# Kernel tuning notes

Measured on AMD Instinct MI355X. Metric: run time of the kernel, lower is better.

## Reference

```python
import jax, jax.numpy as jnp
import numpy as np

NUM_HEADS = 16
EMBED_DIM = 1024
HEAD_DIM = EMBED_DIM // NUM_HEADS


def setup_inputs() -> dict:
    key = jax.random.key(0)
    ks = jax.random.split(key, 9)
    B, S, D = 4, 2048, EMBED_DIM
    scale = 1.0 / np.sqrt(D)
    inp = {
        "x": jax.random.normal(ks[0], (B, S, D), dtype=jnp.float32),
        "Wq": jax.random.normal(ks[1], (D, D), dtype=jnp.float32) * scale,
        "bq": jnp.zeros((D,), dtype=jnp.float32),
        "Wk": jax.random.normal(ks[2], (D, D), dtype=jnp.float32) * scale,
        "bk": jnp.zeros((D,), dtype=jnp.float32),
        "Wv": jax.random.normal(ks[3], (D, D), dtype=jnp.float32) * scale,
        "bv": jnp.zeros((D,), dtype=jnp.float32),
        "Wo": jax.random.normal(ks[4], (D, D), dtype=jnp.float32) * scale,
        "bo": jnp.zeros((D,), dtype=jnp.float32),
    }
    return inp


def reference(x, Wq, bq, Wk, bk, Wv, bv, Wo, bo):
    # x: [B, S, D]; weights stored torch-style as [out, in] -> use x @ W.T + b
    B, S, D = x.shape
    H, Hd = NUM_HEADS, HEAD_DIM

    def proj(W, b):
        return (jnp.einsum('bsd,ed->bse', x, W) + b).reshape(B, S, H, Hd).transpose(0, 2, 1, 3)

    Q = proj(Wq, bq)  # [B, H, S, Hd]
    K = proj(Wk, bk)
    V = proj(Wv, bv)

    scores = jnp.einsum('bhqd,bhkd->bhqk', Q, K) / jnp.sqrt(jnp.float32(Hd))
    attn = jax.nn.softmax(scores, axis=-1)  # dropout is identity in eval mode
    context = jnp.einsum('bhqk,bhkd->bhqd', attn, V)
    context = context.transpose(0, 2, 1, 3).reshape(B, S, D)
    out = jnp.einsum('bsd,ed->bse', context, Wo) + bo
    return out
```

## Files before the change

### kernel.cpp

```cpp
#include <hip/hip_runtime.h>


#define LOG2E 1.4426950408889634f
#define QSCALE (0.125f * LOG2E)

typedef __bf16 bf16x8 __attribute__((ext_vector_type(8)));
typedef float f32x4 __attribute__((ext_vector_type(4)));
typedef float f32x2 __attribute__((ext_vector_type(2)));
typedef unsigned short u16x4 __attribute__((ext_vector_type(4)));
typedef unsigned short u16x8 __attribute__((ext_vector_type(8)));
typedef unsigned int u32x4 __attribute__((ext_vector_type(4)));

__device__ __forceinline__ unsigned short f2bf(float f) {
  unsigned int u = __builtin_bit_cast(unsigned int, f);
  u += 0x7fffu + ((u >> 16) & 1u);
  return (unsigned short)(u >> 16);
}

__device__ __forceinline__ unsigned int cvtpk(float a, float b) {
  unsigned int r;
  asm("v_cvt_pk_bf16_f32 %0, %1, %2" : "=v"(r) : "v"(a), "v"(b));
  return r;
}

typedef const __attribute__((address_space(1))) void* gptr_t;
typedef __attribute__((address_space(3))) void* lptr_t;
__device__ __forceinline__ void gload16(const void* g, void* l) {
  __builtin_amdgcn_global_load_lds((gptr_t)g, (lptr_t)l, 16, 0, 0);
}

__global__ __launch_bounds__(256) void k_cvt(const float* __restrict__ x,
                                             const float* __restrict__ Wq, const float* __restrict__ Wk,
                                             const float* __restrict__ Wv, const float* __restrict__ Wo,
                                             unsigned short* __restrict__ xb, unsigned short* __restrict__ Wb) {
  int gi = (blockIdx.x * 256 + threadIdx.x) * 4;
  if (gi < 8388608) {
    f32x4 v = *(const f32x4*)(x + gi);
    u16x4 o; o[0] = f2bf(v[0]); o[1] = f2bf(v[1]); o[2] = f2bf(v[2]); o[3] = f2bf(v[3]);
    *(u16x4*)(xb + gi) = o;
  } else {
    int i = gi - 8388608;
    int wsel = i >> 20;
    int loc = i & 1048575;
    const float* src = (wsel == 0) ? Wq : (wsel == 1) ? Wk : (wsel == 2) ? Wv : Wo;
    float sc = (wsel == 0) ? QSCALE : 1.0f;
    f32x4 v = *(const f32x4*)(src + loc);
    u16x4 o; o[0] = f2bf(v[0] * sc); o[1] = f2bf(v[1] * sc); o[2] = f2bf(v[2] * sc); o[3] = f2bf(v[3] * sc);
    *(u16x4*)(Wb + i) = o;
  }
}

__global__ __launch_bounds__(256, 3) void k_gemm_qkv(
    const unsigned short* __restrict__ xb, const unsigned short* __restrict__ Wb,
    const float* __restrict__ bq, const float* __restrict__ bk, const float* __restrict__ bv,
    unsigned short* __restrict__ Qb, unsigned short* __restrict__ Kb, unsigned short* __restrict__ Vtb) {
  __shared__ unsigned short As[2 * 4096];
  __shared__ unsigned short Bs[2 * 4096];
  const int tid = threadIdx.x;
  const int lane = tid & 63;
  const int w = tid >> 6;
  const int wm = w & 1;
  const int wn = w >> 1;
  const int lin = blockIdx.x + (blockIdx.y << 3) + (blockIdx.z << 9);
  const int swz = (lin & 7) * 192 + (lin >> 3);
  const int z = swz >> 9;
  const int m0 = ((swz >> 3) & 63) << 7;
  const int n0 = (swz & 7) << 7;
  const unsigned short* W = Wb + ((size_t)z << 20);

  const int sR = tid >> 3;
  const int sc_ = (tid & 7) ^ (sR & 7);
  const int mrow0 = 2 * sR + (sc_ >> 2);
  const int kc0 = (sc_ & 3) << 3;
  const unsigned short* srcA = xb + (size_t)(m0 + mrow0) * 1024 + kc0;
  const unsigned short* srcB = W + (size_t)(n0 + mrow0) * 1024 + kc0;
  unsigned short* dstA = As + tid * 8;
  unsigned short* dstB = Bs + tid * 8;

  const int fr = lane & 15;
  const int kq = lane >> 4;
  int aoff[4], boff[4];
#pragma unroll
  for (int t = 0; t < 4; ++t) {
    int ra = wm * 64 + t * 16 + fr;
    aoff[t] = ((ra >> 1) << 6) + (((((ra & 1) << 2) + kq) ^ ((ra >> 1) & 7)) << 3);
    int rb = wn * 64 + t * 16 + fr;
    boff[t] = ((rb >> 1) << 6) + (((((rb & 1) << 2) + kq) ^ ((rb >> 1) & 7)) << 3);
  }

  const unsigned short* PA = (z == 2) ? As : Bs;
  const unsigned short* PB = (z == 2) ? Bs : As;

  f32x4 zero4 = {0.f, 0.f, 0.f, 0.f};
  f32x4 acc[4][4];
#pragma unroll
  for (int i = 0; i < 4; ++i)
#pragma unroll
    for (int jj = 0; jj < 4; ++jj) acc[i][jj] = zero4;

  gload16(srcA, dstA);
  gload16(srcA + 65536, dstA + 2048);
  gload16(srcB, dstB);
  gload16(srcB + 65536, dstB + 2048);

  int cur = 0;
  for (int kt = 0; kt < 32; ++kt) {
    const int kon = ((kt + 1) & 31) << 5;
    const int soff = (cur ^ 1) << 12;
    gload16(srcA + kon, dstA + soff);
    gload16(srcA + 65536 + kon, dstA + soff + 2048);
    gload16(srcB + kon, dstB + soff);
    gload16(srcB + 65536 + kon, dstB + soff + 2048);

    asm volatile("s_waitcnt vmcnt(4)" ::: "memory");
    __builtin_amdgcn_s_barrier();

    const unsigned short* Ac = PA + (cur << 12);
    const unsigned short* Bc = PB + (cur << 12);
    bf16x8 af[4], bfr[4];
#pragma unroll
    for (int mt = 0; mt < 4; ++mt) af[mt] = *(const bf16x8*)&Ac[aoff[mt]];
#pragma unroll
    for (int nt = 0; nt < 4; ++nt) bfr[nt] = *(const bf16x8*)&Bc[boff[nt]];

    asm volatile("s_waitcnt lgkmcnt(0)" ::: "memory");
    __builtin_amdgcn_s_barrier();

    __builtin_amdgcn_s_setprio(1);
#pragma unroll
    for (int mt = 0; mt < 4; ++mt)
#pragma unroll
      for (int nt = 0; nt < 4; ++nt)
        acc[mt][nt] = __builtin_amdgcn_mfma_f32_16x16x32_bf16(af[mt], bfr[nt], acc[mt][nt], 0, 0, 0);
    __builtin_amdgcn_s_setprio(0);
    cur ^= 1;
  }

  const float* bias = (z == 0) ? bq : (z == 1) ? bk : bv;
  const float bsc = (z == 0) ? QSCALE : 1.0f;
  const int rg = kq << 2;
  if (z == 2) {
#pragma unroll
    for (int mt = 0; mt < 4; ++mt) {
      const int mb = m0 + wm * 64 + mt * 16 + rg;
      const int b = mb >> 11;
      const int s = mb & 2047;
#pragma unroll
      for (int nt = 0; nt < 4; ++nt) {
        const int n = n0 + wn * 64 + nt * 16 + fr;
        const float bvv = bias[n];
        const int h = n >> 6;
        const int d = n & 63;
        u16x4 pk;
#pragma unroll
        for (int r = 0; r < 4; ++r) pk[r] = f2bf(acc[mt][nt][r] + bvv);
        const int pbase = (s & ~31) | ((s & 12) << 1) | ((s & 16) >> 2);
        *(u16x4*)&Vtb[(((size_t)(b * 16 + h) << 6) + d) * 2048 + pbase] = pk;
      }
    }
  } else {
    unsigned short* O = (z == 0) ? Qb : Kb;
#pragma unroll
    for (int mt = 0; mt < 4; ++mt) {
      const int nb = n0 + wm * 64 + mt * 16 + rg;
      const int h = nb >> 6;
      const int dbase = nb & 63;
      f32x4 bv4 = *(const f32x4*)&bias[nb];
#pragma unroll
      for (int r = 0; r < 4; ++r) bv4[r] *= bsc;
#pragma unroll
      for (int nt = 0; nt < 4; ++nt) {
        const int sb = m0 + wn * 64 + nt * 16 + fr;
        const int b = sb >> 11;
        const int s = sb & 2047;
        u16x4 pk;
#pragma unroll
        for (int r = 0; r < 4; ++r) pk[r] = f2bf(acc[mt][nt][r] + bv4[r]);
        *(u16x4*)&O[(((size_t)(b * 16 + h) << 11) + s) * 64 + dbase] = pk;
      }
    }
  }
}

__global__ __launch_bounds__(512, 4) void k_flash(
    const unsigned short* __restrict__ Qb, const unsigned short* __restrict__ Kb,
    const unsigned short* __restrict__ Vtb, unsigned short* __restrict__ Ctx) {
  __shared__ unsigned short Ks[2 * 128 * 64];
  __shared__ unsigned short Vts[2 * 64 * 128];
  const int tid = threadIdx.x;
  const int lane = tid & 63;
  const int wq = tid >> 6;
  const int fr = lane & 15;
  const int qd = lane >> 4;
  const int lin = blockIdx.x + (blockIdx.y << 3);
  const int swz = ((lin & 7) << 6) + (lin >> 3);
  const int bh = swz >> 3;
  const int q0 = (swz & 7) << 8;
  const size_t hoff = (size_t)bh << 17;
  const unsigned short* Qh = Qb + hoff + ((size_t)q0 << 6);

  const unsigned short* kg[2];
  const unsigned short* vg[2];
  unsigned short* kl[2];
  unsigned short* vl[2];
#pragma unroll
  for (int p = 0; p < 2; ++p) {
    int slot = p * 512 + tid;
    int kr = slot >> 3, ch = slot & 7;
    kg[p] = Kb + hoff + (size_t)kr * 64 + ((ch ^ (kr & 7)) << 3);
    kl[p] = Ks + slot * 8;
    int dr = slot >> 4, ch2 = slot & 15;
    vg[p] = Vtb + hoff + (size_t)dr * 2048 + ((ch2 ^ (dr & 15)) << 3);
    vl[p] = Vts + slot * 8;
  }

  int kbase[2];
#pragma unroll
  for (int ds = 0; ds < 2; ++ds)
    kbase[ds] = fr * 64 + (((ds * 4 + qd) ^ (fr & 7)) << 3);
  int vbase[4];
#pragma unroll
  for (int ks = 0; ks < 4; ++ks)
    vbase[ks] = fr * 128 + (((ks * 4 + qd) ^ fr) << 3);

  bf16x8 qf[2][2];
#pragma unroll
  for (int qt = 0; qt < 2; ++qt)
#pragma unroll
    for (int ds = 0; ds < 2; ++ds)
      qf[qt][ds] = *(const bf16x8*)&Qh[(wq * 32 + qt * 16 + fr) * 64 + ds * 32 + qd * 8];

  f32x4 zero4 = {0.f, 0.f, 0.f, 0.f};
  f32x4 o_acc[2][4];
  f32x2 l2[2] = {{0.f, 0.f}, {0.f, 0.f}};
#pragma unroll
  for (int mt = 0; mt < 2; ++mt)
#pragma unroll
    for (int dt = 0; dt < 4; ++dt) o_acc[mt][dt] = zero4;

  gload16(kg[0], kl[0]);
  gload16(kg[1], kl[1]);
  gload16(vg[0], vl[0]);
  gload16(vg[1], vl[1]);

  for (int j = 0; j < 16; ++j) {
    __builtin_amdgcn_s_barrier();
    const int jn = (j + 1) & 15;
    const int sb = ((j + 1) & 1) << 13;
    gload16(kg[0] + jn * 8192, kl[0] + sb);
    gload16(kg[1] + jn * 8192, kl[1] + sb);
    gload16(vg[0] + jn * 128, vl[0] + sb);
    gload16(vg[1] + jn * 128, vl[1] + sb);
    asm volatile("s_waitcnt vmcnt(4)" ::: "memory");
    __builtin_amdgcn_s_barrier();

    const int cb = (j & 1) << 13;
    const unsigned short* Kc = Ks + cb;

    u32x4 pfw[2][4];
#pragma unroll
    for (int ks = 0; ks < 4; ++ks) {
      f32x4 st0[2], st1[2];
      st0[0] = zero4; st0[1] = zero4; st1[0] = zero4; st1[1] = zero4;
      __builtin_amdgcn_s_setprio(1);
#pragma unroll
      for (int ds = 0; ds < 2; ++ds) {
        bf16x8 kf0 = *(const bf16x8*)&Kc[kbase[ds] + (2 * ks) * 1024];
        bf16x8 kf1 = *(const bf16x8*)&Kc[kbase[ds] + (2 * ks + 1) * 1024];
        st0[0] = __builtin_amdgcn_mfma_f32_16x16x32_bf16(kf0, qf[0][ds], st0[0], 0, 0, 0);
        st0[1] = __builtin_amdgcn_mfma_f32_16x16x32_bf16(kf0, qf[1][ds], st0[1], 0, 0, 0);
        st1[0] = __builtin_amdgcn_mfma_f32_16x16x32_bf16(kf1, qf[0][ds], st1[0], 0, 0, 0);
        st1[1] = __builtin_amdgcn_mfma_f32_16x16x32_bf16(kf1, qf[1][ds], st1[1], 0, 0, 0);
      }
      __builtin_amdgcn_s_setprio(0);
#pragma unroll
      for (int mt = 0; mt < 2; ++mt) {
#pragma unroll
        for (int r = 0; r < 4; ++r) {
          st0[mt][r] = __builtin_amdgcn_exp2f(st0[mt][r]);
          st1[mt][r] = __builtin_amdgcn_exp2f(st1[mt][r]);
        }
        f32x2 s01 = {st0[mt][0], st0[mt][1]};
        f32x2 s23 = {st0[mt][2], st0[mt][3]};
        f32x2 t01 = {st1[mt][0], st1[mt][1]};
        f32x2 t23 = {st1[mt][2], st1[mt][3]};
        l2[mt] += (s01 + s23) + (t01 + t23);
        u32x4 pk;
        pk[0] = cvtpk(st0[mt][0], st0[mt][1]);
        pk[1] = cvtpk(st0[mt][2], st0[mt][3]);
        pk[2] = cvtpk(st1[mt][0], st1[mt][1]);
        pk[3] = cvtpk(st1[mt][2], st1[mt][3]);
        pfw[mt][ks] = pk;
      }
    }

    __builtin_amdgcn_s_setprio(1);
#pragma unroll
    for (int ks = 0; ks < 4; ++ks) {
      bf16x8 pf0 = __builtin_bit_cast(bf16x8, pfw[0][ks]);
      bf16x8 pf1 = __builtin_bit_cast(bf16x8, pfw[1][ks]);
#pragma unroll
      for (int dt = 0; dt < 4; ++dt) {
        bf16x8 vf = *(const bf16x8*)&Vts[cb + vbase[ks] + dt * 2048];
        o_acc[0][dt] = __builtin_amdgcn_mfma_f32_16x16x32_bf16(pf0, vf, o_acc[0][dt], 0, 0, 0);
        o_acc[1][dt] = __builtin_amdgcn_mfma_f32_16x16x32_bf16(pf1, vf, o_acc[1][dt], 0, 0, 0);
      }
    }
    __builtin_amdgcn_s_setprio(0);
  }

  float l_red[2];
#pragma unroll
  for (int mt = 0; mt < 2; ++mt) {
    float lv = l2[mt][0] + l2[mt][1];
    lv += __shfl_xor(lv, 16);
    lv += __shfl_xor(lv, 32);
    l_red[mt] = lv;
  }

  const int b = bh >> 4;
  const int h = bh & 15;
#pragma unroll
  for (int mt = 0; mt < 2; ++mt) {
#pragma unroll
    for (int r = 0; r < 4; ++r) {
      float lv = __shfl(l_red[mt], qd * 4 + r);
      float rl = 1.0f / lv;
      int s = q0 + wq * 32 + mt * 16 + qd * 4 + r;
      size_t base = (((size_t)b * 2048 + s) << 10) + (h << 6);
#pragma unroll
      for (int dt = 0; dt < 4; ++dt) Ctx[base + dt * 16 + fr] = f2bf(o_acc[mt][dt][r] * rl);
    }
  }
}

__global__ __launch_bounds__(256, 3) void k_gemm_out(
    const unsigned short* __restrict__ Ctx, const unsigned short* __restrict__ Wo,
    const float* __restrict__ bo, float* __restrict__ out) {
  __shared__ unsigned short As[2 * 4096];
  __shared__ unsigned short Bs[2 * 4096];
  const int tid = threadIdx.x;
  const int lane = tid & 63;
  const int w = tid >> 6;
  const int wm = w & 1;
  const int wn = w >> 1;
  const int lin = blockIdx.x + (blockIdx.y << 3);
  const int swz = ((lin & 7) << 6) + (lin >> 3);
  const int m0 = (swz >> 3) << 7;
  const int n0 = (swz & 7) << 7;

  const int sR = tid >> 3;
  const int sc_ = (tid & 7) ^ (sR & 7);
  const int mrow0 = 2 * sR + (sc_ >> 2);
  const int kc0 = (sc_ & 3) << 3;
  const unsigned short* srcA = Ctx + (size_t)(m0 + mrow0) * 1024 + kc0;
  const unsigned short* srcB = Wo + (size_t)(n0 + mrow0) * 1024 + kc0;
  unsigned short* dstA = As + tid * 8;
  unsigned short* dstB = Bs + tid * 8;

  const int fr = lane & 15;
  const int kq = lane >> 4;
  int aoff[4], boff[4];
#pragma unroll
  for (int t = 0; t < 4; ++t) {
    int ra = wm * 64 + t * 16 + fr;
    aoff[t] = ((ra >> 1) << 6) + (((((ra & 1) << 2) + kq) ^ ((ra >> 1) & 7)) << 3);
    int rb = wn * 64 + t * 16 + fr;
    boff[t] = ((rb >> 1) << 6) + (((((rb & 1) << 2) + kq) ^ ((rb >> 1) & 7)) << 3);
  }

  f32x4 zero4 = {0.f, 0.f, 0.f, 0.f};
  f32x4 acc[4][4];
#pragma unroll
  for (int i = 0; i < 4; ++i)
#pragma unroll
    for (int jj = 0; jj < 4; ++jj) acc[i][jj] = zero4;

  gload16(srcA, dstA);
  gload16(srcA + 65536, dstA + 2048);
  gload16(srcB, dstB);
  gload16(srcB + 65536, dstB + 2048);

  int cur = 0;
  for (int kt = 0; kt < 32; ++kt) {
    const int kon = ((kt + 1) & 31) << 5;
    const int soff = (cur ^ 1) << 12;
    gload16(srcA + kon, dstA + soff);
    gload16(srcA + 65536 + kon, dstA + soff + 2048);
    gload16(srcB + kon, dstB + soff);
    gload16(srcB + 65536 + kon, dstB + soff + 2048);

    asm volatile("s_waitcnt vmcnt(4)" ::: "memory");
    __builtin_amdgcn_s_barrier();

    const unsigned short* Ac = Bs + (cur << 12);
    const unsigned short* Bc = As + (cur << 12);
    bf16x8 af[4], bfr[4];
#pragma unroll
    for (int mt = 0; mt < 4; ++mt) af[mt] = *(const bf16x8*)&Ac[aoff[mt]];
#pragma unroll
    for (int nt = 0; nt < 4; ++nt) bfr[nt] = *(const bf16x8*)&Bc[boff[nt]];

    asm volatile("s_waitcnt lgkmcnt(0)" ::: "memory");
    __builtin_amdgcn_s_barrier();

    __builtin_amdgcn_s_setprio(1);
#pragma unroll
    for (int mt = 0; mt < 4; ++mt)
#pragma unroll
      for (int nt = 0; nt < 4; ++nt)
        acc[mt][nt] = __builtin_amdgcn_mfma_f32_16x16x32_bf16(af[mt], bfr[nt], acc[mt][nt], 0, 0, 0);
    __builtin_amdgcn_s_setprio(0);
    cur ^= 1;
  }

  const int rg = kq << 2;
#pragma unroll
  for (int mt = 0; mt < 4; ++mt) {
    const int nb = n0 + wm * 64 + mt * 16 + rg;
    const f32x4 bv4 = *(const f32x4*)&bo[nb];
#pragma unroll
    for (int nt = 0; nt < 4; ++nt) {
      const int sb = m0 + wn * 64 + nt * 16 + fr;
      f32x4 o = acc[mt][nt] + bv4;
      *(f32x4*)&out[(size_t)sb * 1024 + nb] = o;
    }
  }
}

extern "C" void kernel_launch(void* const* d_in, const int* in_sizes, int n_in,
                              void* d_out, int out_size, void* d_ws, size_t ws_size,
                              hipStream_t stream) {
  (void)in_sizes; (void)n_in; (void)out_size; (void)ws_size;
  const float* x = (const float*)d_in[0];
  const float* Wq = (const float*)d_in[1];
  const float* bq = (const float*)d_in[2];
  const float* Wk = (const float*)d_in[3];
  const float* bk = (const float*)d_in[4];
  const float* Wv = (const float*)d_in[5];
  const float* bv = (const float*)d_in[6];
  const float* Wo = (const float*)d_in[7];
  const float* bo = (const float*)d_in[8];
  float* out = (float*)d_out;

  unsigned short* xb = (unsigned short*)d_ws;
  unsigned short* Wb = xb + 8388608;
  unsigned short* Qb = Wb + 4194304;
  unsigned short* Kb = Qb + 8388608;
  unsigned short* Vtb = Kb + 8388608;
  unsigned short* Ctx = xb;

  k_cvt<<<12288, 256, 0, stream>>>(x, Wq, Wk, Wv, Wo, xb, Wb);
  k_gemm_qkv<<<dim3(8, 64, 3), 256, 0, stream>>>(xb, Wb, bq, bk, bv, Qb, Kb, Vtb);
  k_flash<<<dim3(8, 64), 512, 0, stream>>>(Qb, Kb, Vtb, Ctx);
  k_gemm_out<<<dim3(8, 64), 256, 0, stream>>>(Ctx, Wb + 3 * 1048576, bo, out);
}
```

Baseline: 261.1 us.

## Load V fragments straight from global into registers instead of staging through LDS

The flash attention kernel no longer stages the V^T tile in shared memory. Each wave now reads its V fragments directly from global memory into registers, prefetching the next k-slice while the current P·V MFMAs run. K stays double-buffered in LDS, and the loop now uses a single end-of-iteration vmcnt(0) wait plus barrier instead of two barriers. This halves LDS use and removes a barrier, but every wave now loads the full V tile on its own, which adds cache traffic and exposes global-load latency. The K prefetch no longer wraps its index, so the last iteration reads past the current head's K block.

```diff
diff --git a/kernel.cpp b/kernel.cpp
--- a/kernel.cpp
+++ b/kernel.cpp
@@ -186,7 +186,6 @@
     const unsigned short* __restrict__ Qb, const unsigned short* __restrict__ Kb,
     const unsigned short* __restrict__ Vtb, unsigned short* __restrict__ Ctx) {
   __shared__ unsigned short Ks[2 * 128 * 64];
-  __shared__ unsigned short Vts[2 * 64 * 128];
   const int tid = threadIdx.x;
   const int lane = tid & 63;
   const int wq = tid >> 6;
@@ -200,28 +199,24 @@
   const unsigned short* Qh = Qb + hoff + ((size_t)q0 << 6);
 
   const unsigned short* kg[2];
-  const unsigned short* vg[2];
-  unsigned short* kl[2];
-  unsigned short* vl[2];
+  int klo[2];
 #pragma unroll
   for (int p = 0; p < 2; ++p) {
     int slot = p * 512 + tid;
     int kr = slot >> 3, ch = slot & 7;
     kg[p] = Kb + hoff + (size_t)kr * 64 + ((ch ^ (kr & 7)) << 3);
-    kl[p] = Ks + slot * 8;
-    int dr = slot >> 4, ch2 = slot & 15;
-    vg[p] = Vtb + hoff + (size_t)dr * 2048 + ((ch2 ^ (dr & 15)) << 3);
-    vl[p] = Vts + slot * 8;
+    klo[p] = slot * 8;
   }
 
   int kbase[2];
 #pragma unroll
   for (int ds = 0; ds < 2; ++ds)
     kbase[ds] = fr * 64 + (((ds * 4 + qd) ^ (fr & 7)) << 3);
-  int vbase[4];
-#pragma unroll
-  for (int ks = 0; ks < 4; ++ks)
-    vbase[ks] = fr * 128 + (((ks * 4 + qd) ^ fr) << 3);
+
+  const unsigned short* vgp[4];
+#pragma unroll
+  for (int dt = 0; dt < 4; ++dt)
+    vgp[dt] = Vtb + hoff + (size_t)(dt * 16 + fr) * 2048 + qd * 8;
 
   bf16x8 qf[2][2];
 #pragma unroll
@@ -238,25 +233,18 @@
 #pragma unroll
     for (int dt = 0; dt < 4; ++dt) o_acc[mt][dt] = zero4;
 
-  gload16(kg[0], kl[0]);
-  gload16(kg[1], kl[1]);
-  gload16(vg[0], vl[0]);
-  gload16(vg[1], vl[1]);
-
+  gload16(kg[0], Ks + klo[0]);
+  gload16(kg[1], Ks + klo[1]);
+  kg[0] += 8192; kg[1] += 8192;
+  __syncthreads();
+
+  int curoff = 0;
   for (int j = 0; j < 16; ++j) {
-    __builtin_amdgcn_s_barrier();
-    const int jn = (j + 1) & 15;
-    const int sb = ((j + 1) & 1) << 13;
-    gload16(kg[0] + jn * 8192, kl[0] + sb);
-    gload16(kg[1] + jn * 8192, kl[1] + sb);
-    gload16(vg[0] + jn * 128, vl[0] + sb);
-    gload16(vg[1] + jn * 128, vl[1] + sb);
-    asm volatile("s_waitcnt vmcnt(4)" ::: "memory");
-    __builtin_amdgcn_s_barrier();
-
-    const int cb = (j & 1) << 13;
-    const unsigned short* Kc = Ks + cb;
-
+    gload16(kg[0], Ks + (curoff ^ 8192) + klo[0]);
+    gload16(kg[1], Ks + (curoff ^ 8192) + klo[1]);
+    kg[0] += 8192; kg[1] += 8192;
+
+    const unsigned short* Kc = Ks + curoff;
     u32x4 pfw[2][4];
 #pragma unroll
     for (int ks = 0; ks < 4; ++ks) {
@@ -294,19 +282,35 @@
       }
     }
 
-    __builtin_amdgcn_s_setprio(1);
+    bf16x8 vfa[4], vfb[4];
+#pragma unroll
+    for (int dt = 0; dt < 4; ++dt) vfa[dt] = *(const bf16x8*)(vgp[dt]);
 #pragma unroll
     for (int ks = 0; ks < 4; ++ks) {
+      if (ks < 3) {
+#pragma unroll
+        for (int dt = 0; dt < 4; ++dt) {
+          if (ks & 1) vfa[dt] = *(const bf16x8*)(vgp[dt] + (ks + 1) * 32);
+          else        vfb[dt] = *(const bf16x8*)(vgp[dt] + (ks + 1) * 32);
+        }
+      }
       bf16x8 pf0 = __builtin_bit_cast(bf16x8, pfw[0][ks]);
       bf16x8 pf1 = __builtin_bit_cast(bf16x8, pfw[1][ks]);
+      __builtin_amdgcn_s_setprio(1);
 #pragma unroll
       for (int dt = 0; dt < 4; ++dt) {
-        bf16x8 vf = *(const bf16x8*)&Vts[cb + vbase[ks] + dt * 2048];
+        bf16x8 vf = (ks & 1) ? vfb[dt] : vfa[dt];
         o_acc[0][dt] = __builtin_amdgcn_mfma_f32_16x16x32_bf16(pf0, vf, o_acc[0][dt], 0, 0, 0);
         o_acc[1][dt] = __builtin_amdgcn_mfma_f32_16x16x32_bf16(pf1, vf, o_acc[1][dt], 0, 0, 0);
       }
-    }
-    __builtin_amdgcn_s_setprio(0);
+      __builtin_amdgcn_s_setprio(0);
+    }
+#pragma unroll
+    for (int dt = 0; dt < 4; ++dt) vgp[dt] += 128;
+
+    asm volatile("s_waitcnt vmcnt(0)" ::: "memory");
+    __builtin_amdgcn_s_barrier();
+    curoff ^= 8192;
   }
 
   float l_red[2];
```

Result: slower. 336.8 us (+29.0%).
